# Kernel tuning notes

Measured on AMD Instinct MI355X. Metric: run time of the kernel, lower is better.

The kernel has to match this reference:

```python
import jax, jax.numpy as jnp
import numpy as np

BIG_K, SMALL_K = 13, 3
NK = -(-BIG_K // SMALL_K)  # 5
NUM_PATHS = 3
BN_EPS = 1e-5


def _shifts():
    mid = BIG_K // 2
    pad = SMALL_K - 1
    return [-(mid - i * SMALL_K - pad) for i in range(NK)]  # [-4,-1,2,5,8]


def _conv1x1(x, w):
    return jax.lax.conv_general_dilated(
        x, w, window_strides=(1, 1), padding='VALID',
        dimension_numbers=('NCHW', 'OIHW', 'NCHW'))


def _dwconv3x3(x, w, groups):
    # x: (b, groups, h, w); w: (groups, 1, 3, 3)
    return jax.lax.conv_general_dilated(
        x, w, window_strides=(1, 1), padding=[(1, 1), (1, 1)],
        dimension_numbers=('NCHW', 'OIHW', 'NCHW'),
        feature_group_count=groups)


def setup_inputs() -> dict:
    key = jax.random.key(0)
    ks = jax.random.split(key, 8)
    b, c1, c2, h, w = 16, 256, 256, 64, 64
    return {
        'x': jax.random.normal(ks[0], (b, c1, h, w), jnp.float32),
        'w_expand': jax.random.normal(ks[1], (c2 * NK, c1, 1, 1), jnp.float32) * 0.05,
        'w_path': jax.random.normal(ks[2], (NUM_PATHS, NK, c2, 1, 3, 3), jnp.float32) * 0.1,
        'w_mix': jax.random.normal(ks[3], (c2, c2, 1, 1), jnp.float32) * 0.05,
        'bn_gamma': jnp.ones((c2,), jnp.float32),
        'bn_beta': jnp.zeros((c2,), jnp.float32),
        'bn_mean': jnp.zeros((c2,), jnp.float32),
        'bn_var': jnp.ones((c2,), jnp.float32),
    }


def reference(x, w_expand, w_path, w_mix, bn_gamma, bn_beta, bn_mean, bn_var):
    b, c1, h, w = x.shape
    c2 = w_mix.shape[0]
    # 1) channel expand: c1 -> c2*nk (1x1 conv, big GEMM)
    x_exp = _conv1x1(x, w_expand)                      # (b, c2*NK, h, w)
    x_r = x_exp.reshape(b, c2, NK, h, w)
    # 2) roll each shift group; conv is linear in kernel, so summing over the
    #    3 paths of depthwise weights gives identical math to summing outputs.
    shifts = _shifts()
    rolled = jnp.stack(
        [jnp.roll(x_r[:, :, k], (shifts[k], shifts[k]), axis=(2, 3)) for k in range(NK)],
        axis=2)                                        # (b, c2, NK, h, w)
    rolled_flat = rolled.reshape(b, c2 * NK, h, w)      # channel layout: c2-major, nk-minor
    w_eff = jnp.sum(w_path, axis=0)                     # (NK, c2, 1, 3, 3)
    w_flat = jnp.transpose(w_eff, (1, 0, 2, 3, 4)).reshape(c2 * NK, 1, 3, 3)
    conv_out = _dwconv3x3(rolled_flat, w_flat, groups=c2 * NK)
    merged = conv_out.reshape(b, c2, NK, h, w).sum(axis=2)  # sum over shifts (paths already folded)
    # 3) channel mix + BN (inference) + SiLU
    out = _conv1x1(merged, w_mix)
    inv = jax.lax.rsqrt(bn_var + BN_EPS)
    out = (out - bn_mean[None, :, None, None]) * (bn_gamma * inv)[None, :, None, None] + bn_beta[None, :, None, None]
    return out * jax.nn.sigmoid(out)  # SiLU
```

## Files before the change

### kernel.cpp

```cpp
#include <hip/hip_runtime.h>
#include <hip/hip_bf16.h>
#include <math.h>

#define NB   16
#define C1   256
#define C2   256
#define NK   5
#define NEXP (C2 * NK)
#define HW   4096

typedef __attribute__((ext_vector_type(8))) short bf16x8;
typedef __attribute__((ext_vector_type(4))) float f32x4;

#define GLOAD_LDS16(g, l) __builtin_amdgcn_global_load_lds( \
    (const __attribute__((address_space(1))) void*)(g), \
    (__attribute__((address_space(3))) void*)(l), 16, 0, 0)

__device__ __forceinline__ unsigned short bfbits(float v) {
    return __builtin_bit_cast(unsigned short, __float2bfloat16(v));
}
__device__ __forceinline__ float bflo(unsigned u) { return __uint_as_float(u << 16); }
__device__ __forceinline__ float bfhi(unsigned u) { return __uint_as_float(u & 0xffff0000u); }

#define LGKM_BARRIER() do { \
    asm volatile("s_waitcnt lgkmcnt(0)" ::: "memory"); \
    __builtin_amdgcn_sched_barrier(0); \
    __builtin_amdgcn_s_barrier(); } while (0)

__global__ void weff_kernel(const float* __restrict__ w_path, float* __restrict__ weff) {
    int idx = blockIdx.x * 256 + threadIdx.x;
    if (idx >= NK * C2 * 9) return;
    float s = 0.f;
    #pragma unroll
    for (int p = 0; p < 3; ++p)
        s += w_path[(long)p * NK * C2 * 9 + idx];
    weff[idx] = s;
}

__global__ void cvt_bf16_kernel(const float* __restrict__ in, __hip_bfloat16* __restrict__ out, int n) {
    int i = blockIdx.x * 256 + threadIdx.x;
    if (i < n) out[i] = __float2bfloat16(in[i]);
}

template <int NCH, bool FP32B, bool OUT_BF16>
__global__ __launch_bounds__(512, 2)
void nstream_gemm_kernel(const __hip_bfloat16* __restrict__ A,
                         const void* __restrict__ B_all,
                         void* __restrict__ C_all,
                         long bStrideB, long bStrideC, int bOffB, int bOffC,
                         const float* __restrict__ bn_gamma, const float* __restrict__ bn_beta,
                         const float* __restrict__ bn_mean, const float* __restrict__ bn_var) {
    constexpr int KK = 256, NN = 4096;
    __shared__ __align__(16) char Bs[2][64 * 512];
    const int z  = blockIdx.z;
    const int nBase = blockIdx.x * (64 * NCH);
    const int m0 = blockIdx.y * 256;
    const int t  = threadIdx.x;
    const int lane = t & 63;
    const int wv = t >> 6;
    const int lr = lane & 15, lg = lane >> 4;

    bf16x8 af[2][8];
    const __hip_bfloat16* wp = A + (long)(m0 + wv * 32 + lr) * KK + lg * 8;
    #pragma unroll
    for (int s = 0; s < 2; ++s)
        #pragma unroll
        for (int ks = 0; ks < 8; ++ks)
            af[s][ks] = *(const bf16x8*)(wp + (long)s * 16 * KK + ks * 32);

    float scl[2], mnv[2], btv[2];
    if constexpr (!OUT_BF16) {
        #pragma unroll
        for (int s = 0; s < 2; ++s) {
            const int m = m0 + wv * 32 + s * 16 + lr;
            scl[s] = bn_gamma[m] * rsqrtf(bn_var[m] + 1e-5f);
            mnv[s] = bn_mean[m];
            btv[s] = bn_beta[m];
        }
    }

    const int sn = t & 63;
    const int kb = (t >> 6) * 32;
    const int key = sn & 31;
    const char* Bbase = (const char*)B_all + (long)(bOffB + z) * bStrideB * (FP32B ? 4 : 2);

    float    fr[32];
    unsigned hr[32];

    auto issueB = [&](int ci) {
        const int nc = nBase + ci * 64 + sn;
        #pragma unroll
        for (int gq = 0; gq < 2; ++gq) {
            if constexpr (FP32B) {
                const float* p = (const float*)Bbase + (long)(kb + gq * 16) * NN + nc;
                #pragma unroll
                for (int i = 0; i < 16; ++i) fr[gq * 16 + i] = p[(long)i * NN];
            } else {
                const unsigned short* p = (const unsigned short*)Bbase + (long)(kb + gq * 16) * NN + nc;
                #pragma unroll
                for (int i = 0; i < 16; ++i) hr[gq * 16 + i] = p[(long)i * NN];
            }
        }
    };
    auto writeB = [&](int ci) {
        char* buf = Bs[ci & 1];
        #pragma unroll
        for (int gq = 0; gq < 2; ++gq) {
            unsigned u[8];
            #pragma unroll
            for (int i = 0; i < 8; ++i) {
                if constexpr (FP32B)
                    u[i] = (unsigned)bfbits(fr[gq * 16 + 2 * i]) |
                           ((unsigned)bfbits(fr[gq * 16 + 2 * i + 1]) << 16);
                else
                    u[i] = (hr[gq * 16 + 2 * i] & 0xffffu) | (hr[gq * 16 + 2 * i + 1] << 16);
            }
            const int ch0 = (kb >> 3) + gq * 2;
            *(uint4*)(buf + sn * 512 + ((ch0 ^ key) * 16))       = *(uint4*)&u[0];
            *(uint4*)(buf + sn * 512 + (((ch0 + 1) ^ key) * 16)) = *(uint4*)&u[4];
        }
    };

    issueB(0);
    writeB(0);
    LGKM_BARRIER();

    #pragma unroll
    for (int ci = 0; ci < NCH; ++ci) {
        if (ci + 1 < NCH) {
            issueB(ci + 1);
            __builtin_amdgcn_sched_barrier(0);
        }
        char* buf = Bs[ci & 1];

        f32x4 acc[2][4];
        #pragma unroll
        for (int s = 0; s < 2; ++s)
            #pragma unroll
            for (int j = 0; j < 4; ++j)
                acc[s][j] = (f32x4){0.f, 0.f, 0.f, 0.f};

        __builtin_amdgcn_s_setprio(1);
        #pragma unroll
        for (int ks = 0; ks < 8; ++ks) {
            #pragma unroll
            for (int j = 0; j < 4; ++j) {
                const int n = j * 16 + lr;
                bf16x8 bfr = *(const bf16x8*)(buf + n * 512 + (((ks * 4 + lg) ^ (n & 31)) * 16));
                acc[0][j] = __builtin_amdgcn_mfma_f32_16x16x32_bf16(bfr, af[0][ks], acc[0][j], 0, 0, 0);
                acc[1][j] = __builtin_amdgcn_mfma_f32_16x16x32_bf16(bfr, af[1][ks], acc[1][j], 0, 0, 0);
            }
        }
        __builtin_amdgcn_s_setprio(0);

        const int ncb = nBase + ci * 64;
        if constexpr (OUT_BF16) {
            if (ci + 1 < NCH) writeB(ci + 1);
            __hip_bfloat16* C = (__hip_bfloat16*)C_all + (long)(bOffC + z) * bStrideC;
            #pragma unroll
            for (int s = 0; s < 2; ++s) {
                const int m = m0 + wv * 32 + s * 16 + lr;
                #pragma unroll
                for (int j = 0; j < 4; ++j) {
                    const long n = ncb + j * 16 + lg * 4;
                    short4 sv;
                    sv.x = (short)bfbits(acc[s][j][0]);
                    sv.y = (short)bfbits(acc[s][j][1]);
                    sv.z = (short)bfbits(acc[s][j][2]);
                    sv.w = (short)bfbits(acc[s][j][3]);
                    *(short4*)(C + (long)m * NN + n) = sv;
                }
            }
            if (ci + 1 < NCH) LGKM_BARRIER();
        } else {
            float* C = (float*)C_all + (long)(bOffC + z) * bStrideC;
            LGKM_BARRIER();
            #pragma unroll
            for (int h = 0; h < 2; ++h) {
                if ((wv >> 2) == h) {
                    #pragma unroll
                    for (int s = 0; s < 2; ++s) {
                        const int mrel = (wv & 3) * 32 + s * 16 + lr;
                        const int kx = (mrel & 7) << 4;
                        #pragma unroll
                        for (int j = 0; j < 4; ++j) {
                            const int nb = j * 64 + lg * 16;
                            float4 v;
                            float t0 = (acc[s][j][0] - mnv[s]) * scl[s] + btv[s];
                            float t1 = (acc[s][j][1] - mnv[s]) * scl[s] + btv[s];
                            float t2 = (acc[s][j][2] - mnv[s]) * scl[s] + btv[s];
                            float t3 = (acc[s][j][3] - mnv[s]) * scl[s] + btv[s];
                            v.x = t0 / (1.0f + __expf(-t0));
                            v.y = t1 / (1.0f + __expf(-t1));
                            v.z = t2 / (1.0f + __expf(-t2));
                            v.w = t3 / (1.0f + __expf(-t3));
                            *(float4*)(buf + mrel * 256 + (nb ^ kx)) = v;
                        }
                    }
                }
                LGKM_BARRIER();
                #pragma unroll
                for (int i = 0; i < 4; ++i) {
                    const int p = i * 8192 + t * 16;
                    const int mrel = p >> 8;
                    const int w = p & 255;
                    uint4 v = *(uint4*)(buf + mrel * 256 + (w ^ ((mrel & 7) << 4)));
                    *(uint4*)((char*)(C + (long)(m0 + h * 128 + mrel) * NN + ncb) + w) = v;
                }
                LGKM_BARRIER();
            }
            if (ci + 1 < NCH) {
                writeB(ci + 1);
                LGKM_BARRIER();
            }
        }
    }
}

__global__ __launch_bounds__(512)
void shift_dw_kernel(const __hip_bfloat16* __restrict__ xexp,
                     const float* __restrict__ weff,
                     __hip_bfloat16* __restrict__ merged) {
    __shared__ __align__(16) __hip_bfloat16 sd[NK * 66 * 64];
    const int t = threadIdx.x;
    const int c = blockIdx.x;
    const int z = blockIdx.y;
    const int shifts[NK] = {-4, -1, 2, 5, 8};
    const __hip_bfloat16* base = xexp + ((long)z * NEXP + (long)c * NK) * HW;

    if (t < 80) {
        const int k = t >> 4, which = (t >> 3) & 1, ch = (t & 7) * 8;
        bf16x8 zz = {};
        *(bf16x8*)&sd[(k * 66 + which * 65) * 64 + ch] = zz;
    }
    #pragma unroll
    for (int k = 0; k < NK; ++k) {
        const int r  = t >> 3;
        const int ch = (t & 7) * 8;
        const int grow = (r - shifts[k]) & 63;
        GLOAD_LDS16(base + (long)k * HW + grow * 64 + ch,
                    (char*)sd + (k * 66 + 1) * 128 + t * 16);
    }
    __syncthreads();

    const int pairi = t & 31;
    const int j2 = pairi * 2;
    const int ty = t >> 5;
    const int pbase = ty * 4;

    f32x4 acc[2];
    acc[0] = (f32x4){0.f, 0.f, 0.f, 0.f};
    acc[1] = (f32x4){0.f, 0.f, 0.f, 0.f};

    #pragma unroll
    for (int k = 0; k < NK; ++k) {
        const int s = shifts[k];
        const float* wpk = &weff[((long)k * C2 + c) * 9];
        float wA[9], wB[9];
        #pragma unroll
        for (int i = 0; i < 9; ++i) { wA[i] = wpk[i]; wB[i] = wA[i]; }
        if (j2 == 0)      { wA[0] = 0.f; wA[3] = 0.f; wA[6] = 0.f; }
        if (j2 + 1 == 63) { wB[2] = 0.f; wB[5] = 0.f; wB[8] = 0.f; }
        const int cin = (j2 - 1 - s) & 63;
        const __hip_bfloat16* sdk = sd + k * (66 * 64);

        float V0[4], V1[4], V2[4], V3[4];
        auto LDR = [&](int rs, int slot) {
            const __hip_bfloat16* rp = sdk + (pbase + rs) * 64;
            if ((cin & 1) == 0) {
                unsigned a = *(const unsigned*)(rp + cin);
                unsigned b = *(const unsigned*)(rp + ((cin + 2) & 63));
                V0[slot] = bflo(a); V1[slot] = bfhi(a);
                V2[slot] = bflo(b); V3[slot] = bfhi(b);
            } else {
                unsigned a = *(const unsigned*)(rp + (cin & 62));
                unsigned b = *(const unsigned*)(rp + ((cin + 1) & 63));
                unsigned d = *(const unsigned*)(rp + ((cin + 3) & 63));
                V0[slot] = bfhi(a);
                V1[slot] = bflo(b); V2[slot] = bfhi(b);
                V3[slot] = bflo(d);
            }
        };

        LDR(0, 0); LDR(1, 1); LDR(2, 2); LDR(3, 3);
        #pragma unroll
        for (int pr = 0; pr < 2; ++pr) {
            #pragma unroll
            for (int u = 0; u < 3; ++u) {
                const int iA = (2 * pr + u) & 3;
                const int iB = (2 * pr + u + 1) & 3;
                acc[pr][0] += wA[u*3] * V0[iA] + wA[u*3+1] * V1[iA] + wA[u*3+2] * V2[iA];
                acc[pr][1] += wB[u*3] * V1[iA] + wB[u*3+1] * V2[iA] + wB[u*3+2] * V3[iA];
                acc[pr][2] += wA[u*3] * V0[iB] + wA[u*3+1] * V1[iB] + wA[u*3+2] * V2[iB];
                acc[pr][3] += wB[u*3] * V1[iB] + wB[u*3+1] * V2[iB] + wB[u*3+2] * V3[iB];
            }
            if (pr == 0) { LDR(4, 0); LDR(5, 1); }
        }
    }

    __hip_bfloat16* out = merged + ((long)z * C2 + c) * HW + (long)pbase * 64 + j2;
    #pragma unroll
    for (int pr = 0; pr < 2; ++pr) {
        unsigned ua = (unsigned)bfbits(acc[pr][0]) | ((unsigned)bfbits(acc[pr][1]) << 16);
        unsigned ub = (unsigned)bfbits(acc[pr][2]) | ((unsigned)bfbits(acc[pr][3]) << 16);
        *(unsigned*)(out + (long)(2 * pr) * 64)     = ua;
        *(unsigned*)(out + (long)(2 * pr + 1) * 64) = ub;
    }
}

extern "C" void kernel_launch(void* const* d_in, const int* in_sizes, int n_in,
                              void* d_out, int out_size, void* d_ws, size_t ws_size,
                              hipStream_t stream) {
    const float* x        = (const float*)d_in[0];
    const float* w_expand = (const float*)d_in[1];
    const float* w_path   = (const float*)d_in[2];
    const float* w_mix    = (const float*)d_in[3];
    const float* bn_gamma = (const float*)d_in[4];
    const float* bn_beta  = (const float*)d_in[5];
    const float* bn_mean  = (const float*)d_in[6];
    const float* bn_var   = (const float*)d_in[7];

    char* ws = (char*)d_ws;
    float* weff             = (float*)ws;
    __hip_bfloat16* wexp_bf = (__hip_bfloat16*)(ws + 65536);
    __hip_bfloat16* wmix_bf = (__hip_bfloat16*)(ws + 65536 + 655360);
    const size_t head = 1 << 20;

    const size_t xe_per = (size_t)NEXP * HW * 2;
    const size_t mg_per = (size_t)C2 * HW * 2;
    const size_t per_b = xe_per + mg_per;

    int g = 1;
    if (ws_size > head + per_b) {
        size_t fit = (ws_size - head) / per_b;
        g = (int)(fit < NB ? fit : NB);
        if (g < 1) g = 1;
    }

    char* p = ws + head;
    __hip_bfloat16* xexp   = (__hip_bfloat16*)p; p += (size_t)g * xe_per;
    __hip_bfloat16* merged = (__hip_bfloat16*)p;

    weff_kernel<<<(NK * C2 * 9 + 255) / 256, 256, 0, stream>>>(w_path, weff);
    cvt_bf16_kernel<<<(NEXP * C1 + 255) / 256, 256, 0, stream>>>(w_expand, wexp_bf, NEXP * C1);
    cvt_bf16_kernel<<<(C2 * C2 + 255) / 256, 256, 0, stream>>>(w_mix, wmix_bf, C2 * C2);

    for (int b0 = 0; b0 < NB; b0 += g) {
        int gb = (NB - b0) < g ? (NB - b0) : g;
        nstream_gemm_kernel<4, true, true><<<dim3(HW / 256, NEXP / 256, gb), 512, 0, stream>>>(
            wexp_bf, x, xexp,
            (long)C1 * HW, (long)NEXP * HW, b0, 0,
            nullptr, nullptr, nullptr, nullptr);
        shift_dw_kernel<<<dim3(C2, gb), 512, 0, stream>>>(xexp, weff, merged);
        nstream_gemm_kernel<2, false, false><<<dim3(HW / 128, 1, gb), 512, 0, stream>>>(
            wmix_bf, merged, d_out,
            (long)C2 * HW, (long)C2 * HW, 0, b0,
            bn_gamma, bn_beta, bn_mean, bn_var);
    }
}
```

Measured before the change: 201.3 us.

## Split depthwise shift kernel into half-image row tiles with halo loads

The shift+depthwise kernel now processes 32 rows per block with 256 threads instead of the full 64-row image with 512 threads. The grid doubles to two row tiles per channel. Each tile loads a 34-row halo, including wrapped rows, into a smaller LDS buffer and zeroes the image-boundary rows in registers. This is meant to raise occupancy and block-level parallelism via smaller LDS and blocks, at the cost of loading halo rows twice and adding edge-condition logic.

```diff
diff --git a/kernel.cpp b/kernel.cpp
--- a/kernel.cpp
+++ b/kernel.cpp
@@ -217,29 +217,28 @@
     }
 }
 
-__global__ __launch_bounds__(512)
+__global__ __launch_bounds__(256)
 void shift_dw_kernel(const __hip_bfloat16* __restrict__ xexp,
                      const float* __restrict__ weff,
                      __hip_bfloat16* __restrict__ merged) {
-    __shared__ __align__(16) __hip_bfloat16 sd[NK * 66 * 64];
-    const int t = threadIdx.x;
-    const int c = blockIdx.x;
-    const int z = blockIdx.y;
+    __shared__ __align__(16) __hip_bfloat16 sd[NK * 34 * 64];
+    const int t  = threadIdx.x;
+    const int r0 = blockIdx.x * 32;
+    const int c  = blockIdx.y;
+    const int z  = blockIdx.z;
     const int shifts[NK] = {-4, -1, 2, 5, 8};
     const __hip_bfloat16* base = xexp + ((long)z * NEXP + (long)c * NK) * HW;
 
-    if (t < 80) {
-        const int k = t >> 4, which = (t >> 3) & 1, ch = (t & 7) * 8;
-        bf16x8 zz = {};
-        *(bf16x8*)&sd[(k * 66 + which * 65) * 64 + ch] = zz;
-    }
-    #pragma unroll
-    for (int k = 0; k < NK; ++k) {
-        const int r  = t >> 3;
-        const int ch = (t & 7) * 8;
-        const int grow = (r - shifts[k]) & 63;
-        GLOAD_LDS16(base + (long)k * HW + grow * 64 + ch,
-                    (char*)sd + (k * 66 + 1) * 128 + t * 16);
+    #pragma unroll
+    for (int i = 0; i < 6; ++i) {
+        const int idx = t + i * 256;
+        if (idx < NK * 34 * 8) {
+            const int k   = idx / 272;
+            const int rem = idx - k * 272;
+            const int rr  = rem >> 3, ch = (rem & 7) * 8;
+            const int grow = (r0 - 1 + rr - shifts[k]) & 63;
+            GLOAD_LDS16(base + (long)k * HW + grow * 64 + ch, (char*)sd + idx * 16);
+        }
     }
     __syncthreads();
 
@@ -247,6 +246,8 @@
     const int j2 = pairi * 2;
     const int ty = t >> 5;
     const int pbase = ty * 4;
+    const bool topEdge = (r0 == 0)  && (ty == 0);
+    const bool botEdge = (r0 == 32) && (ty == 7);
 
     f32x4 acc[2];
     acc[0] = (f32x4){0.f, 0.f, 0.f, 0.f};
@@ -262,7 +263,7 @@
         if (j2 == 0)      { wA[0] = 0.f; wA[3] = 0.f; wA[6] = 0.f; }
         if (j2 + 1 == 63) { wB[2] = 0.f; wB[5] = 0.f; wB[8] = 0.f; }
         const int cin = (j2 - 1 - s) & 63;
-        const __hip_bfloat16* sdk = sd + k * (66 * 64);
+        const __hip_bfloat16* sdk = sd + k * (34 * 64);
 
         float V0[4], V1[4], V2[4], V3[4];
         auto LDR = [&](int rs, int slot) {
@@ -283,6 +284,7 @@
         };
 
         LDR(0, 0); LDR(1, 1); LDR(2, 2); LDR(3, 3);
+        if (topEdge) { V0[0] = 0.f; V1[0] = 0.f; V2[0] = 0.f; V3[0] = 0.f; }
         #pragma unroll
         for (int pr = 0; pr < 2; ++pr) {
             #pragma unroll
@@ -294,11 +296,14 @@
                 acc[pr][2] += wA[u*3] * V0[iB] + wA[u*3+1] * V1[iB] + wA[u*3+2] * V2[iB];
                 acc[pr][3] += wB[u*3] * V1[iB] + wB[u*3+1] * V2[iB] + wB[u*3+2] * V3[iB];
             }
-            if (pr == 0) { LDR(4, 0); LDR(5, 1); }
-        }
-    }
-
-    __hip_bfloat16* out = merged + ((long)z * C2 + c) * HW + (long)pbase * 64 + j2;
+            if (pr == 0) {
+                LDR(4, 0); LDR(5, 1);
+                if (botEdge) { V0[1] = 0.f; V1[1] = 0.f; V2[1] = 0.f; V3[1] = 0.f; }
+            }
+        }
+    }
+
+    __hip_bfloat16* out = merged + ((long)z * C2 + c) * HW + (long)(r0 + pbase) * 64 + j2;
     #pragma unroll
     for (int pr = 0; pr < 2; ++pr) {
         unsigned ua = (unsigned)bfbits(acc[pr][0]) | ((unsigned)bfbits(acc[pr][1]) << 16);
@@ -351,7 +356,7 @@
             wexp_bf, x, xexp,
             (long)C1 * HW, (long)NEXP * HW, b0, 0,
             nullptr, nullptr, nullptr, nullptr);
-        shift_dw_kernel<<<dim3(C2, gb), 512, 0, stream>>>(xexp, weff, merged);
+        shift_dw_kernel<<<dim3(2, C2, gb), 256, 0, stream>>>(xexp, weff, merged);
         nstream_gemm_kernel<2, false, false><<<dim3(HW / 128, 1, gb), 512, 0, stream>>>(
             wmix_bf, merged, d_out,
             (long)C2 * HW, (long)C2 * HW, 0, b0,
```

Result: slower. 216.6 us (+7.6%).
